# Kernel tuning notes

Hardware: AMD Instinct MI355X
Metric: run time of the kernel (lower is better)

Reference implementation:

```python
import jax, jax.numpy as jnp
import numpy as np

B, S, DM = 4, 2048, 1024
H, D = 16, 64  # nb_head, size_per_head
NEG = 1e12


def setup_inputs() -> dict:
    key = jax.random.key(0)
    ks = jax.random.split(key, 8)
    return {
        "Q_seq": jax.random.normal(ks[0], (B, S, DM), dtype=jnp.float32),
        "K_seq": jax.random.normal(ks[1], (B, S, DM), dtype=jnp.float32),
        "V_seq": jax.random.normal(ks[2], (B, S, DM), dtype=jnp.float32),
        "Q_len": jax.random.randint(ks[3], (B, 1), 0, S, dtype=jnp.int32),
        "V_len": jax.random.randint(ks[4], (B, 1), 0, S, dtype=jnp.int32),
        "WQ": jax.random.normal(ks[5], (DM, H * D), dtype=jnp.float32) * 0.02,
        "WK": jax.random.normal(ks[6], (DM, H * D), dtype=jnp.float32) * 0.02,
        "WV": jax.random.normal(ks[7], (DM, H * D), dtype=jnp.float32) * 0.02,
    }


def reference(Q_seq, K_seq, V_seq, Q_len, V_len, WQ, WK, WV):
    b, sq, _ = Q_seq.shape
    sk = K_seq.shape[1]
    # project and split heads -> [B, H, S, D]
    q = (Q_seq @ WQ).reshape(b, sq, H, D).transpose(0, 2, 1, 3)
    k = (K_seq @ WK).reshape(b, sk, H, D).transpose(0, 2, 1, 3)
    v = (V_seq @ WV).reshape(b, sk, H, D).transpose(0, 2, 1, 3)
    # scores [B, H, Sq, Sk]
    A = jnp.einsum("bhqd,bhkd->bhqk", q, k) / jnp.sqrt(jnp.float32(D))
    # key-length mask: positions t < V_len are valid (1 - cumsum(one_hot))
    kmask = (jnp.arange(sk)[None, :] < V_len[:, 0:1]).astype(A.dtype)  # [B, Sk]
    A = A - (1.0 - kmask)[:, None, None, :] * NEG
    A = jax.nn.softmax(A, axis=-1)
    O = jnp.einsum("bhqk,bhkd->bhqd", A, v)
    O = O.transpose(0, 2, 1, 3).reshape(b, sq, H * D)
    # query-length mask (multiplicative)
    qmask = (jnp.arange(sq)[None, :] < Q_len[:, 0:1]).astype(O.dtype)  # [B, Sq]
    return O * qmask[:, :, None]
```

## Files before the change

kernel.cpp:

```cpp
#include <hip/hip_runtime.h>
#include <hip/hip_bf16.h>
#include <math.h>

#define BATCH 4
#define SEQ   2048
#define DM    1024
#define NHEAD 16
#define HDIM  64
#define MROWS (BATCH*SEQ)

typedef float f32x4 __attribute__((ext_vector_type(4)));
typedef float f32x16 __attribute__((ext_vector_type(16)));
typedef short bf16x8 __attribute__((ext_vector_type(8)));
typedef unsigned int u32x4 __attribute__((ext_vector_type(4)));

typedef __attribute__((address_space(1))) unsigned int as1_u32;
typedef __attribute__((address_space(3))) unsigned int as3_u32;

__device__ __forceinline__ void gld16(const void* g, void* l) {
    __builtin_amdgcn_global_load_lds((const as1_u32*)g, (as3_u32*)l, 16, 0, 0);
}

__device__ __forceinline__ unsigned short f2bf(float f) {
    unsigned int u = __float_as_uint(f);
    u += 0x7FFFu + ((u >> 16) & 1u);
    return (unsigned short)(u >> 16);
}

__device__ __forceinline__ unsigned int pack2bf(float a, float b) {
    return (unsigned int)f2bf(a) | ((unsigned int)f2bf(b) << 16);
}

__device__ __forceinline__ float fexp2(float x) {
    float r;
    asm("v_exp_f32 %0, %1" : "=v"(r) : "v"(x));
    return r;
}

__device__ __forceinline__ unsigned int cvtpk2(float lo, float hi) {
    unsigned int r;
    asm("v_cvt_pk_bf16_f32 %0, %1, %2" : "=v"(r) : "v"(lo), "v"(hi));
    return r;
}

__device__ __forceinline__ int row_limit(int len, int lmode) {
    if (lmode == 0) return (len + 31) & ~31;
    if (lmode == 1) return (len <= 0) ? 0 : ((len + 63) & ~63);
    return (len <= 0) ? SEQ : ((len + 63) & ~63);
}

__global__ __launch_bounds__(256) void convx3_kernel(const float* __restrict__ Q,
                                                     const float* __restrict__ K,
                                                     const float* __restrict__ V,
                                                     unsigned short* __restrict__ Xq,
                                                     unsigned short* __restrict__ Xk,
                                                     unsigned short* __restrict__ Xv,
                                                     const int* __restrict__ Qlen,
                                                     const int* __restrict__ Vlen,
                                                     int zoff) {
    const int z = blockIdx.y + zoff;
    const float* in = (z == 0) ? Q : (z == 1) ? K : V;
    unsigned short* out = (z == 0) ? Xq : (z == 1) ? Xk : Xv;
    int i = blockIdx.x * 256 + threadIdx.x;
    int row = i >> 7;
    int b = row >> 11, s = row & 2047;
    int lim = (z == 0) ? row_limit(Qlen[b], 0) : row_limit(Vlen[b], z);
    if (s >= lim) return;
    const float4* p = reinterpret_cast<const float4*>(in) + (size_t)i * 2;
    float4 a = p[0], v = p[1];
    uint4 r;
    r.x = pack2bf(a.x, a.y);
    r.y = pack2bf(a.z, a.w);
    r.z = pack2bf(v.x, v.y);
    r.w = pack2bf(v.z, v.w);
    reinterpret_cast<uint4*>(out)[i] = r;
}

__global__ __launch_bounds__(256) void convw3_kernel(const float* __restrict__ WQ,
                                                     const float* __restrict__ WK,
                                                     const float* __restrict__ WV,
                                                     unsigned short* __restrict__ Oq,
                                                     unsigned short* __restrict__ Ok,
                                                     unsigned short* __restrict__ Ov,
                                                     int zoff) {
    const int z = blockIdx.z + zoff;
    const float* in = (z == 0) ? WQ : (z == 1) ? WK : WV;
    unsigned short* out = (z == 0) ? Oq : (z == 1) ? Ok : Ov;
    const float scale = (z == 0) ? 0.125f * 1.44269504088896340736f : 1.0f;
    __shared__ float tile[64][65];
    int n0 = blockIdx.x * 64, k0 = blockIdx.y * 64;
    int tx = threadIdx.x, ty = threadIdx.y;
#pragma unroll
    for (int i = 0; i < 64; i += 4)
        tile[ty + i][tx] = in[(size_t)(k0 + ty + i) * DM + n0 + tx];
    __syncthreads();
#pragma unroll
    for (int i = 0; i < 64; i += 4)
        out[(size_t)(n0 + ty + i) * DM + k0 + tx] = f2bf(tile[tx][ty + i] * scale);
}

__global__ __launch_bounds__(256) void gemm3_kernel(const unsigned short* __restrict__ Xq,
                                                    const unsigned short* __restrict__ Xk,
                                                    const unsigned short* __restrict__ Xv,
                                                    const unsigned short* __restrict__ Wq,
                                                    const unsigned short* __restrict__ Wk,
                                                    const unsigned short* __restrict__ Wv,
                                                    unsigned short* __restrict__ qo,
                                                    unsigned short* __restrict__ ko,
                                                    unsigned short* __restrict__ vo,
                                                    const int* __restrict__ Qlen,
                                                    const int* __restrict__ Vlen,
                                                    int zoff) {
    const int z = blockIdx.z + zoff;
    const unsigned short* A = (z == 0) ? Xq : (z == 1) ? Xk : Xv;
    const unsigned short* Bt = (z == 0) ? Wq : (z == 1) ? Wk : Wv;
    unsigned short* out = (z == 0) ? qo : (z == 1) ? ko : vo;
    const int vmode = (z == 2);
    const int mt_ = (blockIdx.y >> 3) * 8 + blockIdx.x;
    const int nt_ = blockIdx.y & 7;
    const int m0 = mt_ << 7, n0 = nt_ << 7;
    {
        int b = m0 >> 11, s0 = m0 & 2047;
        int len = (z == 0) ? Qlen[b] : Vlen[b];
        if (s0 >= row_limit(len, z)) return;
    }
    __shared__ unsigned short lA[2][128 * 32];
    __shared__ unsigned short lB[2][128 * 32];
    const int tid = threadIdx.x, lane = tid & 63, wave = tid >> 6;
    const int wr = wave >> 1, wc = wave & 1;
    const int col = lane & 15, grp = lane >> 4;

    f32x4 acc[4][4] = {};

    const int srow = tid >> 2, sseg = tid & 3;
    const unsigned short* srcA0 = A + (size_t)(m0 + srow) * DM + sseg * 8;
    const unsigned short* srcA1 = srcA0 + (size_t)64 * DM;
    const unsigned short* srcB0 = Bt + (size_t)(n0 + srow) * DM + sseg * 8;
    const unsigned short* srcB1 = srcB0 + (size_t)64 * DM;

#define STAGEG(BF, K0) do {                                   \
        gld16(srcA0 + (K0), &lA[BF][wave * 512]);             \
        gld16(srcA1 + (K0), &lA[BF][2048 + wave * 512]);      \
        gld16(srcB0 + (K0), &lB[BF][wave * 512]);             \
        gld16(srcB1 + (K0), &lB[BF][2048 + wave * 512]);      \
    } while (0)

    STAGEG(0, 0);
    __syncthreads();

    int bf = 0;
    for (int k0 = 0; k0 < DM; k0 += 32) {
        if (k0 + 32 < DM) STAGEG(bf ^ 1, k0 + 32);

        bf16x8 af[4], bfr[4];
#pragma unroll
        for (int mt = 0; mt < 4; mt++)
            af[mt] = *reinterpret_cast<const bf16x8*>(&lA[bf][(wr * 64 + mt * 16 + col) * 32 + grp * 8]);
#pragma unroll
        for (int nt = 0; nt < 4; nt++)
            bfr[nt] = *reinterpret_cast<const bf16x8*>(&lB[bf][(wc * 64 + nt * 16 + col) * 32 + grp * 8]);
#pragma unroll
        for (int mt = 0; mt < 4; mt++)
#pragma unroll
            for (int nt = 0; nt < 4; nt++)
                acc[mt][nt] = __builtin_amdgcn_mfma_f32_16x16x32_bf16(af[mt], bfr[nt], acc[mt][nt], 0, 0, 0);

        __syncthreads();
        bf ^= 1;
    }
#undef STAGEG

#pragma unroll
    for (int mt = 0; mt < 4; mt++) {
        int rowb = m0 + wr * 64 + mt * 16 + grp * 4;
#pragma unroll
        for (int nt = 0; nt < 4; nt++) {
            int c = n0 + wc * 64 + nt * 16 + col;
            int h = c >> 6, d = c & 63;
            if (vmode == 0) {
#pragma unroll
                for (int r = 0; r < 4; r++) {
                    int rr = rowb + r;
                    int b = rr >> 11, s = rr & 2047;
                    out[((((size_t)(b * NHEAD + h)) << 11) + s) * HDIM + d] = f2bf(acc[mt][nt][r]);
                }
            } else {
                int b = rowb >> 11, s = rowb & 2047;
                uint2 pk;
                pk.x = pack2bf(acc[mt][nt][0], acc[mt][nt][1]);
                pk.y = pack2bf(acc[mt][nt][2], acc[mt][nt][3]);
                *reinterpret_cast<uint2*>(
                    &out[(((size_t)(b * NHEAD + h)) * HDIM + d) * SEQ + s]) = pk;
            }
        }
    }
}

__global__ __launch_bounds__(512) void flash_kernel(const unsigned short* __restrict__ qm,
                                                    const unsigned short* __restrict__ km,
                                                    const unsigned short* __restrict__ vtm,
                                                    const int* __restrict__ Qlen,
                                                    const int* __restrict__ Vlen,
                                                    float* __restrict__ out) {
    const int raw = blockIdx.x;
    const int x = raw & 7, y = raw >> 3;
    const int qt = y & 15, z = y >> 4;
    const int h = x + ((z & 1) << 3);
    const int b = z >> 1;
    const int q0 = qt << 7;
    const int lane = threadIdx.x & 63, wv = threadIdx.x >> 6;
    const int qw = wv & 3, kw = wv >> 2;
    const int qI = lane & 31, hi = lane >> 5;
    const int ql = Qlen[b], vl = Vlen[b];
    const int qrow = q0 + qw * 32 + qI;

    if (q0 >= ql) {
        int r = threadIdx.x >> 2;
        int c0 = (threadIdx.x & 3) * 16;
        float* p = out + (size_t)(b * SEQ + q0 + r) * DM + h * HDIM + c0;
        float4 z4 = {0.f, 0.f, 0.f, 0.f};
        reinterpret_cast<float4*>(p)[0] = z4;
        reinterpret_cast<float4*>(p)[1] = z4;
        reinterpret_cast<float4*>(p)[2] = z4;
        reinterpret_cast<float4*>(p)[3] = z4;
        return;
    }

    const bool uniform = (vl <= 0);
    const int eff = uniform ? SEQ : vl;
    const int nkv = (eff + 63) >> 6;

    const size_t hb = ((size_t)(b * NHEAD + h)) << 11;
    const unsigned short* qbase = qm + hb * HDIM;
    const unsigned short* kbase = km + hb * HDIM;
    const unsigned short* vbase = vtm + hb * HDIM;

    __shared__ __align__(16) unsigned short lsK[2][2][64 * 64];
    __shared__ __align__(16) unsigned short lsV[2][2][64 * 64];

    const int r8 = lane >> 3, cs = lane & 7;
    const int sx = cs ^ r8;
    const size_t offK0 = (size_t)(qw * 16 + r8) * HDIM + sx * 8;
    const size_t offK1 = offK0 + (size_t)8 * HDIM;
    const size_t offV0 = (size_t)(qw * 16 + r8) * SEQ + sx * 8;
    const size_t offV1 = offV0 + (size_t)8 * SEQ;

#define STAGE(BF, T) do {                                                \
        const int kv0_ = (T) << 6;                                       \
        const unsigned short* gk_ = kbase + (size_t)kv0_ * HDIM;         \
        const unsigned short* gv_ = vbase + kv0_;                        \
        gld16(gk_ + offK0, &lsK[kw][BF][(qw * 16) * 64]);                \
        gld16(gk_ + offK1, &lsK[kw][BF][(qw * 16 + 8) * 64]);            \
        gld16(gv_ + offV0, &lsV[kw][BF][(qw * 16) * 64]);                \
        gld16(gv_ + offV1, &lsV[kw][BF][(qw * 16 + 8) * 64]);            \
    } while (0)

    bf16x8 qB[4];
#pragma unroll
    for (int sp = 0; sp < 4; sp++)
        qB[sp] = *reinterpret_cast<const bf16x8*>(&qbase[(size_t)qrow * HDIM + sp * 16 + hi * 8]);

    f32x16 o_acc2[2] = {};
    float m = -3.0e38f, l = 0.f;
    const int q7 = qI & 7;

    const int rounds = (nkv + 1) >> 1;
    if (kw < nkv) STAGE(0, kw);
    __syncthreads();

    int bf = 0;
    for (int r = 0; r < rounds; r++) {
        const int tcur = 2 * r + kw;
        const int tnext = tcur + 2;
        if (tnext < nkv) STAGE(bf ^ 1, tnext);

        if (tcur < nkv) {
            const int kv0 = tcur << 6;

            f32x16 st2[2] = {};
            const unsigned short* Kb = &lsK[kw][bf][0];
#pragma unroll
            for (int kt = 0; kt < 2; kt++)
#pragma unroll
                for (int sp = 0; sp < 4; sp++) {
                    int xs = (sp * 2 + hi) ^ q7;
                    bf16x8 ka = *reinterpret_cast<const bf16x8*>(&Kb[(kt * 32 + qI) * 64 + xs * 8]);
                    st2[kt] = __builtin_amdgcn_mfma_f32_32x32x16_bf16(ka, qB[sp], st2[kt], 0, 0, 0);
                }

            if (uniform) {
#pragma unroll
                for (int t = 0; t < 2; t++)
#pragma unroll
                    for (int rr = 0; rr < 16; rr++) st2[t][rr] = 0.f;
            } else if (kv0 + 64 > eff) {
#pragma unroll
                for (int t = 0; t < 2; t++)
#pragma unroll
                    for (int rr = 0; rr < 16; rr++)
                        if (kv0 + t * 32 + (rr & 3) + 8 * (rr >> 2) + 4 * hi >= eff)
                            st2[t][rr] = -1e30f;
            }

            float tm8[8];
#pragma unroll
            for (int rr = 0; rr < 8; rr++)
                tm8[rr] = fmaxf(fmaxf(st2[0][rr], st2[0][rr + 8]), fmaxf(st2[1][rr], st2[1][rr + 8]));
            float tm4[4];
#pragma unroll
            for (int rr = 0; rr < 4; rr++) tm4[rr] = fmaxf(tm8[rr], tm8[rr + 4]);
            float mx = fmaxf(fmaxf(tm4[0], tm4[1]), fmaxf(tm4[2], tm4[3]));
            mx = fmaxf(mx, __shfl_xor(mx, 32));
            if (!__all(mx - m <= 8.0f)) {
                float mnew = fmaxf(m, mx);
                float sc = fexp2(m - mnew);
                l *= sc;
                o_acc2[0] *= sc;
                o_acc2[1] *= sc;
                m = mnew;
            }
#pragma unroll
            for (int t = 0; t < 2; t++)
#pragma unroll
                for (int rr = 0; rr < 16; rr++) st2[t][rr] = fexp2(st2[t][rr] - m);
            float ts8[8];
#pragma unroll
            for (int rr = 0; rr < 8; rr++)
                ts8[rr] = (st2[0][rr] + st2[0][rr + 8]) + (st2[1][rr] + st2[1][rr + 8]);
            float ts4[4];
#pragma unroll
            for (int rr = 0; rr < 4; rr++) ts4[rr] = ts8[rr] + ts8[rr + 4];
            float rs = (ts4[0] + ts4[1]) + (ts4[2] + ts4[3]);
            rs += __shfl_xor(rs, 32);
            l += rs;

            unsigned int pk[2][8];
#pragma unroll
            for (int t = 0; t < 2; t++)
#pragma unroll
                for (int p = 0; p < 8; p++)
                    pk[t][p] = cvtpk2(st2[t][2 * p], st2[t][2 * p + 1]);

            const unsigned short* Vb = &lsV[kw][bf][0];
#pragma unroll
            for (int ks = 0; ks < 4; ks++) {
                const int t = ks >> 1, c = (ks & 1) * 4;
                unsigned int sel0 = pk[t][c], sel1 = pk[t][c + 1];
                unsigned int sel2 = pk[t][c + 2], sel3 = pk[t][c + 3];
                unsigned int sendA = hi ? sel0 : sel2;
                unsigned int sendB = hi ? sel1 : sel3;
                unsigned int gotA = __shfl_xor(sendA, 32);
                unsigned int gotB = __shfl_xor(sendB, 32);
                u32x4 u;
                u[0] = hi ? gotA : sel0;
                u[1] = hi ? gotB : sel1;
                u[2] = hi ? sel2 : gotA;
                u[3] = hi ? sel3 : gotB;
                bf16x8 pB = __builtin_bit_cast(bf16x8, u);
                int xs = (ks * 2 + hi) ^ q7;
#pragma unroll
                for (int dt = 0; dt < 2; dt++) {
                    bf16x8 va = *reinterpret_cast<const bf16x8*>(&Vb[(dt * 32 + qI) * 64 + xs * 8]);
                    o_acc2[dt] = __builtin_amdgcn_mfma_f32_32x32x16_bf16(va, pB, o_acc2[dt], 0, 0, 0);
                }
            }
        }

        __syncthreads();
        bf ^= 1;
    }
#undef STAGE

    float* osc = (float*)&lsK[0][0][0];
    float* mls = (float*)&lsV[0][0][0];
    const int self = (wv << 6) + lane;
    const int peer = ((wv ^ 4) << 6) + lane;
    f32x16 o_keep = (kw == 0) ? o_acc2[0] : o_acc2[1];
    f32x16 o_give = (kw == 0) ? o_acc2[1] : o_acc2[0];
    mls[self * 2] = m;
    mls[self * 2 + 1] = l;
#pragma unroll
    for (int i = 0; i < 16; i++) osc[self * 16 + i] = o_give[i];
    __syncthreads();
    const float m2 = mls[peer * 2], l2 = mls[peer * 2 + 1];
    const float msh = fmaxf(m, m2);
    const float f1 = fexp2(m - msh), f2 = fexp2(m2 - msh);
    const float rl = 1.0f / (f1 * l + f2 * l2);
    const bool live = (qrow < ql);
    float* obase = out + (size_t)(b * SEQ + qrow) * DM + h * HDIM;
#pragma unroll
    for (int a = 0; a < 4; a++) {
        float4 val;
        float v0 = f1 * o_keep[4 * a + 0] + f2 * osc[peer * 16 + 4 * a + 0];
        float v1 = f1 * o_keep[4 * a + 1] + f2 * osc[peer * 16 + 4 * a + 1];
        float v2 = f1 * o_keep[4 * a + 2] + f2 * osc[peer * 16 + 4 * a + 2];
        float v3 = f1 * o_keep[4 * a + 3] + f2 * osc[peer * 16 + 4 * a + 3];
        val.x = live ? v0 * rl : 0.f;
        val.y = live ? v1 * rl : 0.f;
        val.z = live ? v2 * rl : 0.f;
        val.w = live ? v3 * rl : 0.f;
        *reinterpret_cast<float4*>(&obase[kw * 32 + a * 8 + hi * 4]) = val;
    }
}

extern "C" void kernel_launch(void* const* d_in, const int* in_sizes, int n_in,
                              void* d_out, int out_size, void* d_ws, size_t ws_size,
                              hipStream_t stream) {
    const float* Q_seq = (const float*)d_in[0];
    const float* K_seq = (const float*)d_in[1];
    const float* V_seq = (const float*)d_in[2];
    const int* Q_len = (const int*)d_in[3];
    const int* V_len = (const int*)d_in[4];
    const float* WQ = (const float*)d_in[5];
    const float* WK = (const float*)d_in[6];
    const float* WV = (const float*)d_in[7];
    float* out = (float*)d_out;

    const size_t XN = (size_t)MROWS * DM;
    const size_t WN = (size_t)DM * DM;
    const size_t need_fast = (6 * XN + 3 * WN) * sizeof(unsigned short);

    const int cx_grid = MROWS * DM / 8 / 256;
    dim3 cw_grid(DM / 64, DM / 64, 3), cw_blk(64, 4);
    dim3 g_grid(8, 64, 3), g_blk(256);

    if (ws_size >= need_fast) {
        unsigned short* Xq = (unsigned short*)d_ws;
        unsigned short* Xk = Xq + XN;
        unsigned short* Xv = Xk + XN;
        unsigned short* Wq = Xv + XN;
        unsigned short* Wk = Wq + WN;
        unsigned short* Wv = Wk + WN;
        unsigned short* qb = Wv + WN;
        unsigned short* kb = qb + XN;
        unsigned short* vtb = kb + XN;

        convx3_kernel<<<dim3(cx_grid, 3), 256, 0, stream>>>(Q_seq, K_seq, V_seq,
                                                            Xq, Xk, Xv, Q_len, V_len, 0);
        convw3_kernel<<<cw_grid, cw_blk, 0, stream>>>(WQ, WK, WV, Wq, Wk, Wv, 0);
        gemm3_kernel<<<g_grid, g_blk, 0, stream>>>(Xq, Xk, Xv, Wq, Wk, Wv,
                                                   qb, kb, vtb, Q_len, V_len, 0);
        flash_kernel<<<dim3(1024), 512, 0, stream>>>(qb, kb, vtb, Q_len, V_len, out);
    } else {
        unsigned short* Xbuf = (unsigned short*)d_ws;
        unsigned short* Wt = Xbuf + XN;
        unsigned short* qb = Wt + WN;
        unsigned short* kb = qb + XN;
        unsigned short* vtb = kb + XN;
        dim3 cw1(DM / 64, DM / 64, 1);
        dim3 g1(8, 64, 1);
        for (int z = 0; z < 3; z++) {
            convx3_kernel<<<dim3(cx_grid, 1), 256, 0, stream>>>(Q_seq, K_seq, V_seq,
                                                                Xbuf, Xbuf, Xbuf, Q_len, V_len, z);
            convw3_kernel<<<cw1, cw_blk, 0, stream>>>(WQ, WK, WV, Wt, Wt, Wt, z);
            gemm3_kernel<<<g1, g_blk, 0, stream>>>(Xbuf, Xbuf, Xbuf, Wt, Wt, Wt,
                                                   qb, kb, vtb, Q_len, V_len, z);
        }
        flash_kernel<<<dim3(1024), 512, 0, stream>>>(qb, kb, vtb, Q_len, V_len, out);
    }
}
```

Before: 136.3 us.

## Load projection GEMM fragments directly from global memory, dropping LDS staging

The QKV projection GEMM no longer stages A and B tiles through LDS with async global-to-LDS loads and barriers. Each lane now loads its MFMA fragments straight from global memory into registers, prefetching the next k-slice while the current one is multiplied. This removes LDS traffic and the per-iteration block barrier, but loses reuse across waves, so each tile row is fetched several times from global/L2 with narrow strided accesses, and register pressure rises.

```diff
diff --git a/kernel.cpp b/kernel.cpp
--- a/kernel.cpp
+++ b/kernel.cpp
@@ -124,51 +124,49 @@
         int len = (z == 0) ? Qlen[b] : Vlen[b];
         if (s0 >= row_limit(len, z)) return;
     }
-    __shared__ unsigned short lA[2][128 * 32];
-    __shared__ unsigned short lB[2][128 * 32];
-    const int tid = threadIdx.x, lane = tid & 63, wave = tid >> 6;
+    const int lane = threadIdx.x & 63, wave = threadIdx.x >> 6;
     const int wr = wave >> 1, wc = wave & 1;
     const int col = lane & 15, grp = lane >> 4;
 
     f32x4 acc[4][4] = {};
 
-    const int srow = tid >> 2, sseg = tid & 3;
-    const unsigned short* srcA0 = A + (size_t)(m0 + srow) * DM + sseg * 8;
-    const unsigned short* srcA1 = srcA0 + (size_t)64 * DM;
-    const unsigned short* srcB0 = Bt + (size_t)(n0 + srow) * DM + sseg * 8;
-    const unsigned short* srcB1 = srcB0 + (size_t)64 * DM;
-
-#define STAGEG(BF, K0) do {                                   \
-        gld16(srcA0 + (K0), &lA[BF][wave * 512]);             \
-        gld16(srcA1 + (K0), &lA[BF][2048 + wave * 512]);      \
-        gld16(srcB0 + (K0), &lB[BF][wave * 512]);             \
-        gld16(srcB1 + (K0), &lB[BF][2048 + wave * 512]);      \
-    } while (0)
-
-    STAGEG(0, 0);
-    __syncthreads();
-
-    int bf = 0;
+    const unsigned short* aAddr[4];
+    const unsigned short* bAddr[4];
+#pragma unroll
+    for (int mt = 0; mt < 4; mt++)
+        aAddr[mt] = A + (size_t)(m0 + wr * 64 + mt * 16 + col) * DM + grp * 8;
+#pragma unroll
+    for (int nt = 0; nt < 4; nt++)
+        bAddr[nt] = Bt + (size_t)(n0 + wc * 64 + nt * 16 + col) * DM + grp * 8;
+
+    bf16x8 af[4], bfr[4];
+#pragma unroll
+    for (int mt = 0; mt < 4; mt++) af[mt] = *reinterpret_cast<const bf16x8*>(aAddr[mt]);
+#pragma unroll
+    for (int nt = 0; nt < 4; nt++) bfr[nt] = *reinterpret_cast<const bf16x8*>(bAddr[nt]);
+
     for (int k0 = 0; k0 < DM; k0 += 32) {
-        if (k0 + 32 < DM) STAGEG(bf ^ 1, k0 + 32);
-
-        bf16x8 af[4], bfr[4];
-#pragma unroll
-        for (int mt = 0; mt < 4; mt++)
-            af[mt] = *reinterpret_cast<const bf16x8*>(&lA[bf][(wr * 64 + mt * 16 + col) * 32 + grp * 8]);
-#pragma unroll
-        for (int nt = 0; nt < 4; nt++)
-            bfr[nt] = *reinterpret_cast<const bf16x8*>(&lB[bf][(wc * 64 + nt * 16 + col) * 32 + grp * 8]);
+        bf16x8 naf[4], nbf[4];
+        if (k0 + 32 < DM) {
+#pragma unroll
+            for (int mt = 0; mt < 4; mt++)
+                naf[mt] = *reinterpret_cast<const bf16x8*>(aAddr[mt] + k0 + 32);
+#pragma unroll
+            for (int nt = 0; nt < 4; nt++)
+                nbf[nt] = *reinterpret_cast<const bf16x8*>(bAddr[nt] + k0 + 32);
+        }
 #pragma unroll
         for (int mt = 0; mt < 4; mt++)
 #pragma unroll
             for (int nt = 0; nt < 4; nt++)
                 acc[mt][nt] = __builtin_amdgcn_mfma_f32_16x16x32_bf16(af[mt], bfr[nt], acc[mt][nt], 0, 0, 0);
-
-        __syncthreads();
-        bf ^= 1;
-    }
-#undef STAGEG
+        if (k0 + 32 < DM) {
+#pragma unroll
+            for (int mt = 0; mt < 4; mt++) af[mt] = naf[mt];
+#pragma unroll
+            for (int nt = 0; nt < 4; nt++) bfr[nt] = nbf[nt];
+        }
+    }
 
 #pragma unroll
     for (int mt = 0; mt < 4; mt++) {
```

Measured after the change: 223.2 us. +63.8%, slower.
